# Optimization experiments

Measured on AMD Instinct MI355X. Metric: run time of the kernel, lower is better.

Reference implementation:

```python
import jax, jax.numpy as jnp
import numpy as np
import math

INF = 1e10

def setup_inputs() -> dict:
    key = jax.random.key(0)
    ks = jax.random.split(key, 6)
    B, S, T, D = 8, 1024, 1024, 1024
    stdv = 1.0 / math.sqrt(D)
    return {
        "key": jax.random.normal(ks[0], (B, S, D), dtype=jnp.float32),
        "mask_src": jnp.ones((B, S), dtype=jnp.float32),
        "mask_trg": jnp.ones((B, T), dtype=jnp.float32),
        "Wq": jax.random.uniform(ks[1], (D, D), jnp.float32, -stdv, stdv),
        "bq": jnp.zeros((D,), jnp.float32),
        "Wk": jax.random.uniform(ks[2], (D, D), jnp.float32, -stdv, stdv),
        "bk": jnp.zeros((D,), jnp.float32),
        "wg": jax.random.uniform(ks[3], (D,), jnp.float32, -stdv, stdv),
        "bg": jnp.zeros((1,), jnp.float32),
    }


def reference(key, mask_src, mask_trg, Wq, bq, Wk, bk, wg, bg):
    B, S, D = key.shape
    T = mask_trg.shape[1]
    scale = jnp.asarray(math.sqrt(D), key.dtype)

    # --- linear (position-based Gaussian) attention ---
    src_lens = mask_src.sum(-1)                      # [B]
    trg_lens = mask_trg.sum(-1)                      # [B]
    steps = src_lens / trg_lens                      # [B]
    idx_t = steps[:, None] * jnp.arange(T, dtype=key.dtype)[None, :]   # [B,T]
    idx_s = jnp.arange(S, dtype=key.dtype)                              # [S]
    dist2 = (idx_s[None, None, :] - idx_t[:, :, None]) ** 2            # [B,T,S]
    l_logits = -dist2 / 0.3 - INF * (1.0 - mask_src[:, None, :])
    l_att = jax.nn.softmax(l_logits, axis=-1)                           # [B,T,S]

    # query from position attention
    query = jnp.einsum('bts,bsd->btd', l_att, key)                      # [B,T,D]

    # learned gate, broadcast [B,T,1] -> [B,T,S]
    gates = jax.nn.sigmoid(query @ wg + bg)[:, :, None]                 # [B,T,1]

    # QK dot-product attention
    q = query @ Wq.T + bq                                               # [B,T,D]
    k = key @ Wk.T + bk                                                 # [B,S,D]
    dots = jnp.einsum('btd,bsd->bts', q, k)
    dots = dots - (1.0 - mask_src[:, None, :]) * INF
    probs = jax.nn.softmax(dots / scale, axis=-1)                       # [B,T,S]

    # gated mixture of QK attention and position attention
    return (1.0 - gates) * probs + gates * l_att
```

## Files before the change

### kernel.cpp

```cpp
#include <hip/hip_runtime.h>
#include <hip/hip_bf16.h>
#include <stdint.h>

typedef unsigned short ushort_t;

#define BB 8
#define SS 1024
#define TT 1024
#define DD 1024
#define INF_ 1e10f

__device__ __forceinline__ float b2f(ushort_t u){
  union { unsigned u32; float f; } x; x.u32 = ((unsigned)u) << 16; return x.f;
}
__device__ __forceinline__ ushort_t f2b(float f){
  union { float f; unsigned u; } x; x.f = f;
  unsigned r = x.u + 0x7FFFu + ((x.u >> 16) & 1u);
  return (ushort_t)(r >> 16);
}

__global__ __launch_bounds__(256) void pre_kernel(
    const float* __restrict__ Wq, const float* __restrict__ Wk,
    ushort_t* __restrict__ WqT, ushort_t* __restrict__ WkT,
    const float* __restrict__ msrc, const float* __restrict__ mtrg,
    float* __restrict__ steps, float* __restrict__ v2)
{
  __shared__ float tile[32][33];
  __shared__ float sh[8];
  int blk = blockIdx.x, tid = threadIdx.x;
  if (blk < 2048){
    const float* src = (blk >= 1024) ? Wk : Wq;
    ushort_t* dst = (blk >= 1024) ? WkT : WqT;
    int q = blk & 1023;
    int tx = q & 31, ty = q >> 5;
    int c = tid & 31, r0 = tid >> 5;
    #pragma unroll
    for (int k = 0; k < 4; k++){
      int r = r0 + k*8;
      tile[r][c] = src[(size_t)(ty*32 + r)*DD + tx*32 + c];
    }
    __syncthreads();
    #pragma unroll
    for (int k = 0; k < 4; k++){
      int r = r0 + k*8;
      dst[(size_t)(tx*32 + r)*DD + ty*32 + c] = f2b(tile[c][r]);
    }
  } else {
    int b = blk - 2048;
    if (b < 4) v2[b*256 + tid] = 0.f;
    float a = 0.f, c = 0.f;
    for (int i = tid; i < SS; i += 256) a += msrc[b*SS + i];
    for (int i = tid; i < TT; i += 256) c += mtrg[b*TT + i];
    #pragma unroll
    for (int o = 32; o; o >>= 1){ a += __shfl_xor(a, o); c += __shfl_xor(c, o); }
    int wv = tid >> 6, ln = tid & 63;
    if (!ln){ sh[wv] = a; sh[4+wv] = c; }
    __syncthreads();
    if (!tid){
      float sa = sh[0]+sh[1]+sh[2]+sh[3];
      float sc = sh[4]+sh[5]+sh[6]+sh[7];
      steps[b] = sa / sc;
    }
  }
}

__global__ __launch_bounds__(256) void v2_kernel(
    const float* __restrict__ Wk, const float* __restrict__ bq,
    float* __restrict__ v2)
{
  int tid = threadIdx.x;
  int f = tid * 4;
  int r0 = blockIdx.x * 32;
  float a0=0.f, a1=0.f, a2=0.f, a3=0.f;
  for (int r = 0; r < 32; r++){
    float s = bq[r0 + r];
    float4 w = *(const float4*)(Wk + (size_t)(r0 + r)*DD + f);
    a0 += s*w.x; a1 += s*w.y; a2 += s*w.z; a3 += s*w.w;
  }
  atomicAdd(&v2[f+0], a0); atomicAdd(&v2[f+1], a1);
  atomicAdd(&v2[f+2], a2); atomicAdd(&v2[f+3], a3);
}

__global__ __launch_bounds__(256) void key_convert_kernel(
    const float* __restrict__ key, const float* __restrict__ wg,
    const float* __restrict__ v2f, ushort_t* __restrict__ keyb,
    float* __restrict__ kw, float* __restrict__ cv)
{
  __shared__ float sh[8];
  int row = blockIdx.x;
  int tid = threadIdx.x, d0 = tid*4;
  float4 v = *(const float4*)(key + (size_t)row*DD + d0);
  ushort4 o; o.x=f2b(v.x); o.y=f2b(v.y); o.z=f2b(v.z); o.w=f2b(v.w);
  *(ushort4*)(keyb + (size_t)row*DD + d0) = o;
  float4 w4 = *(const float4*)(wg + d0);
  float4 u4 = *(const float4*)(v2f + d0);
  float pk = v.x*w4.x + v.y*w4.y + v.z*w4.z + v.w*w4.w;
  float pc = v.x*u4.x + v.y*u4.y + v.z*u4.z + v.w*u4.w;
  #pragma unroll
  for (int off = 32; off; off >>= 1){ pk += __shfl_xor(pk, off); pc += __shfl_xor(pc, off); }
  int wvv = tid >> 6;
  if ((tid & 63) == 0){ sh[wvv] = pk; sh[4+wvv] = pc; }
  __syncthreads();
  if (!tid){
    kw[row] = sh[0]+sh[1]+sh[2]+sh[3];
    cv[row] = sh[4]+sh[5]+sh[6]+sh[7];
  }
}

typedef __bf16 bf16x8 __attribute__((ext_vector_type(8)));
typedef float f32x4 __attribute__((ext_vector_type(4)));

#define CP16(g, l) __builtin_amdgcn_global_load_lds( \
    (const __attribute__((address_space(1))) void*)(g), \
    (__attribute__((address_space(3))) void*)(l), 16, 0, 0)

__global__ __launch_bounds__(256, 2) void gemm_bt_kernel(
    const ushort_t* __restrict__ A, const ushort_t* __restrict__ Bm,
    const float* __restrict__ bias, void* __restrict__ Cv,
    int M, int N, int K, int lda, int ldb,
    long long sA, long long sB, long long sC, int hasBias, int outBF16,
    int gx, int gxy)
{
  __shared__ ushort_t lA[128*32];
  __shared__ ushort_t lB[128*32];

  const int bpx = gridDim.x >> 3;
  const int lin = blockIdx.x;
  const int glob = (lin & 7) * bpx + (lin >> 3);
  const int bz = glob / gxy;
  const int rem = glob - bz * gxy;
  const int by = rem / gx;
  const int bx = rem - by * gx;

  A  += (size_t)bz * sA;
  Bm += (size_t)bz * sB;

  const int tid = threadIdx.x;
  const int wv = tid >> 6, ln = tid & 63;
  const int r4 = ln >> 2, c8 = (ln & 3) * 8;

  const ushort_t* gA0 = A  + (size_t)(by*128 + wv*32 + r4) * lda + c8;
  const ushort_t* gA1 = gA0 + (size_t)16 * lda;
  const ushort_t* gB0 = Bm + (size_t)(bx*128 + wv*32 + r4) * ldb + c8;
  const ushort_t* gB1 = gB0 + (size_t)16 * ldb;
  ushort_t* lA0 = &lA[(wv*32     ) * 32];
  ushort_t* lA1 = &lA[(wv*32 + 16) * 32];
  ushort_t* lB0 = &lB[(wv*32     ) * 32];
  ushort_t* lB1 = &lB[(wv*32 + 16) * 32];

  const int lm = ln & 15, qd = ln >> 4;
  const int wm = (wv >> 1) * 64, wn = (wv & 1) * 64;

  f32x4 acc[4][4];
  #pragma unroll
  for (int i = 0; i < 4; i++)
    #pragma unroll
    for (int j = 0; j < 4; j++) acc[i][j] = (f32x4){0.f, 0.f, 0.f, 0.f};

  for (int k0 = 0; k0 < K; k0 += 32){
    CP16(gA0, lA0); CP16(gA1, lA1); CP16(gB0, lB0); CP16(gB1, lB1);
    gA0 += 32; gA1 += 32; gB0 += 32; gB1 += 32;
    __syncthreads();
    bf16x8 af[4], bf[4];
    #pragma unroll
    for (int i = 0; i < 4; i++) af[i] = *(const bf16x8*)&lA[(wm + i*16 + lm)*32 + qd*8];
    #pragma unroll
    for (int j = 0; j < 4; j++) bf[j] = *(const bf16x8*)&lB[(wn + j*16 + lm)*32 + qd*8];
    #pragma unroll
    for (int i = 0; i < 4; i++)
      #pragma unroll
      for (int j = 0; j < 4; j++)
        acc[i][j] = __builtin_amdgcn_mfma_f32_16x16x32_bf16(af[i], bf[j], acc[i][j], 0, 0, 0);
    __syncthreads();
  }

  const int row0 = by*128 + wm + qd*4;
  const int col0 = bx*128 + wn + lm;
  ushort_t* Cb = (ushort_t*)Cv + (size_t)bz * sC;
  float*    Cf = (float*)Cv    + (size_t)bz * sC;
  #pragma unroll
  for (int j = 0; j < 4; j++){
    int col = col0 + j*16;
    float bv = hasBias ? bias[col] : 0.f;
    #pragma unroll
    for (int i = 0; i < 4; i++)
      #pragma unroll
      for (int r = 0; r < 4; r++){
        size_t idx = (size_t)(row0 + i*16 + r) * N + col;
        float v = acc[i][j][r] + bv;
        if (outBF16) Cb[idx] = f2b(v); else Cf[idx] = v;
      }
  }
}

#define G2_STAGE_A(sel) do{ \
    ushort_t* _d = &lA3[(sel)*(256*64) + (w*8)*64]; \
    CP16(gA0, _d); \
    CP16(gA1, _d + 64*64); \
    CP16(gA2, _d + 128*64); \
    CP16(gA3, _d + 192*64); }while(0)
#define G2_STAGE_B(sel) do{ \
    ushort_t* _d = &lB3[(sel)*(128*64) + (w*8)*64]; \
    CP16(gB0, _d); \
    CP16(gB1, _d + 64*64); }while(0)
#define G2_ADV() do{ gA0+=64; gA1+=64; gA2+=64; gA3+=64; gB0+=64; gB1+=64; }while(0)
#define BAR()    asm volatile("s_barrier" ::: "memory")
#define LGKM0()  do{ asm volatile("s_waitcnt lgkmcnt(0)" ::: "memory"); \
                     __builtin_amdgcn_sched_barrier(0); }while(0)

__global__ __launch_bounds__(512, 2) void gemm256_kernel(
    const ushort_t* __restrict__ A, const ushort_t* __restrict__ Bm,
    ushort_t* __restrict__ C,
    int M, int N, int K, int lda, int ldb,
    long long sA, long long sB, long long sC, int gx, int gxy)
{
  __shared__ ushort_t lA3[3 * 256 * 64];
  __shared__ ushort_t lB3[3 * 128 * 64];
  (void)M;

  const int bpx = gridDim.x >> 3;
  const int lin = blockIdx.x;
  const int glob = (lin & 7) * bpx + (lin >> 3);
  const int bz = glob / gxy;
  const int rem = glob - bz * gxy;
  const int by = rem / gx;
  const int bx = rem - by * gx;

  A  += (size_t)bz * sA;
  Bm += (size_t)bz * sB;

  const int tid = threadIdx.x;
  const int w = tid >> 6, l = tid & 63;
  const int lm = l & 15, qd = l >> 4;
  const int wm = w >> 2, wn = w & 3;

  const int srow = l >> 3;
  const int sch  = (l & 7) ^ srow;

  const ushort_t* gA0 = A + (size_t)(by*256 +       w*8 + srow) * lda + sch*8;
  const ushort_t* gA1 = gA0 + (size_t)64  * lda;
  const ushort_t* gA2 = gA0 + (size_t)128 * lda;
  const ushort_t* gA3 = gA0 + (size_t)192 * lda;
  const ushort_t* gB0 = Bm + (size_t)(bx*128 +      w*8 + srow) * ldb + sch*8;
  const ushort_t* gB1 = gB0 + (size_t)64  * ldb;

  f32x4 acc[8][2];
  #pragma unroll
  for (int i = 0; i < 8; i++){ acc[i][0] = (f32x4){0.f,0.f,0.f,0.f}; acc[i][1] = (f32x4){0.f,0.f,0.f,0.f}; }

  G2_STAGE_A(0); G2_STAGE_B(0); G2_ADV();
  G2_STAGE_A(1); G2_STAGE_B(1); G2_ADV();
  asm volatile("s_waitcnt vmcnt(6)" ::: "memory");
  BAR();

  const int NT = K >> 6;
  int rd = 0, st = 2;
  #pragma unroll 1
  for (int t = 0; t < NT; ++t){
    const ushort_t* sa = &lA3[rd*(256*64) + (wm*128)*64];
    const ushort_t* sb = &lB3[rd*(128*64) + (wn*32)*64];
    const bool pre = (t + 2 < NT);

    {
      const int ch = qd ^ (lm & 7);
      bf16x8 af[8], bfr[2];
      #pragma unroll
      for (int i = 0; i < 8; i++) af[i]  = *(const bf16x8*)&sa[(i*16 + lm)*64 + ch*8];
      #pragma unroll
      for (int j = 0; j < 2; j++) bfr[j] = *(const bf16x8*)&sb[(j*16 + lm)*64 + ch*8];
      if (pre) G2_STAGE_A(st);
      BAR();
      LGKM0();
      __builtin_amdgcn_s_setprio(1);
      #pragma unroll
      for (int i = 0; i < 8; i++)
        #pragma unroll
        for (int j = 0; j < 2; j++)
          acc[i][j] = __builtin_amdgcn_mfma_f32_16x16x32_bf16(af[i], bfr[j], acc[i][j], 0, 0, 0);
      __builtin_amdgcn_s_setprio(0);
      BAR();
    }
    {
      const int ch = (4 | qd) ^ (lm & 7);
      bf16x8 af[8], bfr[2];
      #pragma unroll
      for (int i = 0; i < 8; i++) af[i]  = *(const bf16x8*)&sa[(i*16 + lm)*64 + ch*8];
      #pragma unroll
      for (int j = 0; j < 2; j++) bfr[j] = *(const bf16x8*)&sb[(j*16 + lm)*64 + ch*8];
      if (pre) G2_STAGE_B(st);
      BAR();
      LGKM0();
      __builtin_amdgcn_s_setprio(1);
      #pragma unroll
      for (int i = 0; i < 8; i++)
        #pragma unroll
        for (int j = 0; j < 2; j++)
          acc[i][j] = __builtin_amdgcn_mfma_f32_16x16x32_bf16(af[i], bfr[j], acc[i][j], 0, 0, 0);
      __builtin_amdgcn_s_setprio(0);
    }
    if (pre) G2_ADV();
    if (t < NT - 1){
      if (pre) asm volatile("s_waitcnt vmcnt(6)" ::: "memory");
      else     asm volatile("s_waitcnt vmcnt(0)" ::: "memory");
      BAR();
    }
    rd = (rd == 2) ? 0 : rd + 1;
    st = (st == 2) ? 0 : st + 1;
  }

  const int row0 = by*256 + wm*128 + qd*4;
  const int col0 = bx*128 + wn*32 + lm;
  ushort_t* Cp = C + (size_t)bz * sC;
  #pragma unroll
  for (int j = 0; j < 2; j++)
    #pragma unroll
    for (int i = 0; i < 8; i++)
      #pragma unroll
      for (int r = 0; r < 4; r++)
        Cp[(size_t)(row0 + i*16 + r) * N + col0 + j*16] = f2b(acc[i][j][r]);
}

__global__ __launch_bounds__(256) void wmt_reduce_kernel(
    const float* __restrict__ part, ushort_t* __restrict__ dst)
{
  int i4 = blockIdx.x * 256 + threadIdx.x;
  const float4* p = (const float4*)part;
  float4 a = p[i4];
  float4 b = p[i4 + 262144];
  float4 c = p[i4 + 524288];
  float4 d = p[i4 + 786432];
  ushort4 o;
  o.x = f2b(a.x + b.x + c.x + d.x);
  o.y = f2b(a.y + b.y + c.y + d.y);
  o.z = f2b(a.z + b.z + c.z + d.z);
  o.w = f2b(a.w + b.w + c.w + d.w);
  ((ushort4*)dst)[i4] = o;
}

__global__ __launch_bounds__(256) void band_kernel(
    const ushort_t* __restrict__ kmb, const float* __restrict__ mask_src,
    const float* __restrict__ steps, const float* __restrict__ kw,
    const float* __restrict__ bg, ushort_t* __restrict__ qm2b,
    float* __restrict__ gates)
{
  __shared__ float shw[8][17];
  __shared__ int shslo[8];
  int bx = blockIdx.x;
  int b = bx >> 7, t0 = (bx & 127) * 8;
  int tid = threadIdx.x;

  if (tid < 8){
    int t = t0 + tid;
    float c = steps[b] * (float)t;
    int slo = (int)ceilf(c - 8.0f);
    float w[17], m = -3e38f;
    #pragma unroll
    for (int i = 0; i < 17; i++){
      int s = slo + i;
      float l = -3e38f;
      if (s >= 0 && s < SS){
        float dd = (float)s - c;
        l = -dd*dd*(1.0f/0.3f) - INF_*(1.0f - mask_src[b*SS + s]);
      }
      w[i] = l; m = fmaxf(m, l);
    }
    float norm = 0.f, ga = 0.f;
    #pragma unroll
    for (int i = 0; i < 17; i++){
      float e = __expf(w[i] - m);
      int s = slo + i;
      if (s >= 0 && s < SS) ga += e * kw[b*SS + s]; else e = 0.f;
      w[i] = e; norm += e;
    }
    float inv = 1.0f / norm;
    #pragma unroll
    for (int i = 0; i < 17; i++) shw[tid][i] = w[i] * inv;
    shslo[tid] = slo;
    gates[b*TT + t] = 1.0f / (1.0f + __expf(-(ga*inv + bg[0])));
  }
  __syncthreads();

  int smin = shslo[0], smax = shslo[7] + 16;
  if (smin < 0) smin = 0;
  if (smax > SS-1) smax = SS-1;
  int d0 = tid * 4;
  float acc[8][4];
  #pragma unroll
  for (int t = 0; t < 8; t++){ acc[t][0]=0.f; acc[t][1]=0.f; acc[t][2]=0.f; acc[t][3]=0.f; }

  const ushort_t* kbase = kmb + ((size_t)b*SS)*DD + d0;
  for (int s = smin; s <= smax; s++){
    ushort4 kv = *(const ushort4*)(kbase + (size_t)s*DD);
    float k0 = b2f(kv.x), k1 = b2f(kv.y), k2 = b2f(kv.z), k3 = b2f(kv.w);
    #pragma unroll
    for (int t = 0; t < 8; t++){
      unsigned u = (unsigned)(s - shslo[t]);
      if (u < 17u){
        float wgt = shw[t][u];
        acc[t][0] += wgt*k0; acc[t][1] += wgt*k1; acc[t][2] += wgt*k2; acc[t][3] += wgt*k3;
      }
    }
  }
  #pragma unroll
  for (int t = 0; t < 8; t++){
    ushort4 o; o.x=f2b(acc[t][0]); o.y=f2b(acc[t][1]); o.z=f2b(acc[t][2]); o.w=f2b(acc[t][3]);
    *(ushort4*)(qm2b + ((size_t)(b*TT + t0 + t))*DD + d0) = o;
  }
}

__device__ __forceinline__ float blkmax(float v, float* sh){
  #pragma unroll
  for (int o = 32; o; o >>= 1) v = fmaxf(v, __shfl_xor(v, o));
  __syncthreads();
  if ((threadIdx.x & 63) == 0) sh[threadIdx.x >> 6] = v;
  __syncthreads();
  return fmaxf(fmaxf(sh[0], sh[1]), fmaxf(sh[2], sh[3]));
}
__device__ __forceinline__ float blksum(float v, float* sh){
  #pragma unroll
  for (int o = 32; o; o >>= 1) v += __shfl_xor(v, o);
  __syncthreads();
  if ((threadIdx.x & 63) == 0) sh[threadIdx.x >> 6] = v;
  __syncthreads();
  return sh[0] + sh[1] + sh[2] + sh[3];
}

__global__ __launch_bounds__(256) void softmax_mix_kernel(
    const ushort_t* __restrict__ dotsb, float* __restrict__ out,
    const float* __restrict__ mask_src, const float* __restrict__ steps,
    const float* __restrict__ gates, const float* __restrict__ cv)
{
  __shared__ float sh[4];
  int blk = blockIdx.x;
  int b = blk >> 10, t = blk & 1023;
  int tid = threadIdx.x;
  int s0 = tid * 4;
  float c = steps[b] * (float)t;

  ushort4 dv = *(const ushort4*)(dotsb + (size_t)blk*SS + s0);
  float4 mv = *(const float4*)(mask_src + (size_t)b*SS + s0);
  float4 cva = *(const float4*)(cv + (size_t)b*SS + s0);
  float dvf[4] = {b2f(dv.x) + cva.x, b2f(dv.y) + cva.y, b2f(dv.z) + cva.z, b2f(dv.w) + cva.w};
  float msk[4] = {mv.x, mv.y, mv.z, mv.w};
  float dl[4], ll[4];
  float dmax = -3e38f, lmax = -3e38f;
  #pragma unroll
  for (int r = 0; r < 4; r++){
    float im = INF_ * (1.0f - msk[r]);
    dl[r] = (dvf[r] - im) * (1.0f/32.0f);
    float dd = (float)(s0 + r) - c;
    ll[r] = -dd*dd*(1.0f/0.3f) - im;
    dmax = fmaxf(dmax, dl[r]);
    lmax = fmaxf(lmax, ll[r]);
  }
  float dm = blkmax(dmax, sh);
  float ps[4], lp[4];
  float psum = 0.f, lsum = 0.f;
  #pragma unroll
  for (int r = 0; r < 4; r++){ ps[r] = __expf(dl[r] - dm); psum += ps[r]; }
  psum = blksum(psum, sh);
  float lm2 = blkmax(lmax, sh);
  #pragma unroll
  for (int r = 0; r < 4; r++){ lp[r] = __expf(ll[r] - lm2); lsum += lp[r]; }
  lsum = blksum(lsum, sh);

  float g = gates[blk];
  float ip = (1.0f - g) / psum, il = g / lsum;
  float4 ov;
  ov.x = ps[0]*ip + lp[0]*il;
  ov.y = ps[1]*ip + lp[1]*il;
  ov.z = ps[2]*ip + lp[2]*il;
  ov.w = ps[3]*ip + lp[3]*il;
  *(float4*)(out + (size_t)blk*SS + s0) = ov;
}

extern "C" void kernel_launch(void* const* d_in, const int* in_sizes, int n_in,
                              void* d_out, int out_size, void* d_ws, size_t ws_size,
                              hipStream_t stream)
{
  const float* key      = (const float*)d_in[0];
  const float* mask_src = (const float*)d_in[1];
  const float* mask_trg = (const float*)d_in[2];
  const float* Wq       = (const float*)d_in[3];
  const float* bq       = (const float*)d_in[4];
  const float* Wk       = (const float*)d_in[5];
  const float* bk       = (const float*)d_in[6];
  const float* wg       = (const float*)d_in[7];
  const float* bg       = (const float*)d_in[8];
  float* out = (float*)d_out;
  (void)bk;

  char* ws = (char*)d_ws;
  float* steps     = (float*)ws;
  float* gates     = (float*)(ws + 4096);
  float* cv        = (float*)(ws + 4096 + 32768);
  float* kw        = (float*)(ws + 4096 + 65536);
  float* v2        = (float*)(ws + 4096 + 98304);
  ushort_t* WqTb   = (ushort_t*)(ws + 131072);
  ushort_t* WkTb   = WqTb + (size_t)DD*DD;
  ushort_t* WmTb   = WkTb + (size_t)DD*DD;
  ushort_t* keyb   = WmTb + (size_t)DD*DD;
  ushort_t* kmb    = keyb + (size_t)BB*SS*DD;
  char* shared16   = (char*)(kmb + (size_t)BB*SS*DD);
  float* wmPart    = (float*)shared16;
  ushort_t* qm2b   = (ushort_t*)shared16;
  ushort_t* dotsb  = kmb;

  pre_kernel<<<2056, 256, 0, stream>>>(Wq, Wk, WqTb, WkTb, mask_src, mask_trg, steps, v2);
  v2_kernel<<<32, 256, 0, stream>>>(Wk, bq, v2);
  key_convert_kernel<<<BB*SS, 256, 0, stream>>>(key, wg, v2, keyb, kw, cv);
  gemm_bt_kernel<<<256, 256, 0, stream>>>(
      WkTb, WqTb, nullptr, (void*)wmPart, DD, DD, DD/4, DD, DD,
      DD/4, DD/4, (long long)DD*DD, 0, 0, 8, 64);
  wmt_reduce_kernel<<<DD*DD/4/256, 256, 0, stream>>>(wmPart, WmTb);
  gemm256_kernel<<<256, 512, 0, stream>>>(
      keyb, WmTb, kmb, BB*SS, DD, DD, DD, DD, 0, 0, 0, 8, 256);
  band_kernel<<<BB*TT/8, 256, 0, stream>>>(kmb, mask_src, steps, kw, bg, qm2b, gates);
  gemm256_kernel<<<256, 512, 0, stream>>>(
      qm2b, keyb, dotsb, TT, SS, DD, DD, DD,
      (long long)TT*DD, (long long)SS*DD, (long long)TT*SS, 8, 32);
  softmax_mix_kernel<<<BB*TT, 256, 0, stream>>>(dotsb, out, mask_src, steps, gates, cv);
}
```

Before: 211.8 us.

## Merge small prep kernels, reorder block mapping, and fuse softmax reductions

```diff
diff --git a/kernel.cpp b/kernel.cpp
--- a/kernel.cpp
+++ b/kernel.cpp
@@ -23,10 +23,12 @@
     const float* __restrict__ Wq, const float* __restrict__ Wk,
     ushort_t* __restrict__ WqT, ushort_t* __restrict__ WkT,
     const float* __restrict__ msrc, const float* __restrict__ mtrg,
-    float* __restrict__ steps, float* __restrict__ v2)
+    float* __restrict__ steps, float* __restrict__ v2,
+    const float* __restrict__ bq)
 {
   __shared__ float tile[32][33];
   __shared__ float sh[8];
+  __shared__ float shv[128];
   int blk = blockIdx.x, tid = threadIdx.x;
   if (blk < 2048){
     const float* src = (blk >= 1024) ? Wk : Wq;
@@ -45,9 +47,8 @@
       int r = r0 + k*8;
       dst[(size_t)(tx*32 + r)*DD + ty*32 + c] = f2b(tile[c][r]);
     }
-  } else {
+  } else if (blk < 2056){
     int b = blk - 2048;
-    if (b < 4) v2[b*256 + tid] = 0.f;
     float a = 0.f, c = 0.f;
     for (int i = tid; i < SS; i += 256) a += msrc[b*SS + i];
     for (int i = tid; i < TT; i += 256) c += mtrg[b*TT + i];
@@ -61,33 +62,43 @@
       float sc = sh[4]+sh[5]+sh[6]+sh[7];
       steps[b] = sa / sc;
     }
-  }
-}
-
-__global__ __launch_bounds__(256) void v2_kernel(
-    const float* __restrict__ Wk, const float* __restrict__ bq,
-    float* __restrict__ v2)
-{
-  int tid = threadIdx.x;
-  int f = tid * 4;
-  int r0 = blockIdx.x * 32;
-  float a0=0.f, a1=0.f, a2=0.f, a3=0.f;
-  for (int r = 0; r < 32; r++){
-    float s = bq[r0 + r];
-    float4 w = *(const float4*)(Wk + (size_t)(r0 + r)*DD + f);
-    a0 += s*w.x; a1 += s*w.y; a2 += s*w.z; a3 += s*w.w;
-  }
-  atomicAdd(&v2[f+0], a0); atomicAdd(&v2[f+1], a1);
-  atomicAdd(&v2[f+2], a2); atomicAdd(&v2[f+3], a3);
+  } else {
+    int b2 = blk - 2056;
+    int fcol = b2*128 + (tid & 127);
+    int half = tid >> 7;
+    float a = 0.f;
+    const float* Wp = Wk + (size_t)(half*512)*DD + fcol;
+    for (int d = 0; d < 512; ++d) a += Wp[(size_t)d*DD] * bq[half*512 + d];
+    if (half == 0) shv[tid] = a;
+    __syncthreads();
+    if (half == 1) v2[fcol] = a + shv[tid & 127];
+  }
 }
 
 __global__ __launch_bounds__(256) void key_convert_kernel(
     const float* __restrict__ key, const float* __restrict__ wg,
     const float* __restrict__ v2f, ushort_t* __restrict__ keyb,
-    float* __restrict__ kw, float* __restrict__ cv)
+    float* __restrict__ kw, float* __restrict__ cv,
+    const float* __restrict__ part, ushort_t* __restrict__ wmt)
 {
   __shared__ float sh[8];
-  int row = blockIdx.x;
+  int blk = blockIdx.x;
+  if (blk >= BB*SS){
+    int i4 = (blk - BB*SS) * 256 + threadIdx.x;
+    const float4* p = (const float4*)part;
+    float4 a = p[i4];
+    float4 b = p[i4 + 262144];
+    float4 c = p[i4 + 524288];
+    float4 d = p[i4 + 786432];
+    ushort4 o;
+    o.x = f2b(a.x + b.x + c.x + d.x);
+    o.y = f2b(a.y + b.y + c.y + d.y);
+    o.z = f2b(a.z + b.z + c.z + d.z);
+    o.w = f2b(a.w + b.w + c.w + d.w);
+    ((ushort4*)wmt)[i4] = o;
+    return;
+  }
+  int row = blk;
   int tid = threadIdx.x, d0 = tid*4;
   float4 v = *(const float4*)(key + (size_t)row*DD + d0);
   ushort4 o; o.x=f2b(v.x); o.y=f2b(v.y); o.z=f2b(v.z); o.w=f2b(v.w);
@@ -320,23 +331,6 @@
         Cp[(size_t)(row0 + i*16 + r) * N + col0 + j*16] = f2b(acc[i][j][r]);
 }
 
-__global__ __launch_bounds__(256) void wmt_reduce_kernel(
-    const float* __restrict__ part, ushort_t* __restrict__ dst)
-{
-  int i4 = blockIdx.x * 256 + threadIdx.x;
-  const float4* p = (const float4*)part;
-  float4 a = p[i4];
-  float4 b = p[i4 + 262144];
-  float4 c = p[i4 + 524288];
-  float4 d = p[i4 + 786432];
-  ushort4 o;
-  o.x = f2b(a.x + b.x + c.x + d.x);
-  o.y = f2b(a.y + b.y + c.y + d.y);
-  o.z = f2b(a.z + b.z + c.z + d.z);
-  o.w = f2b(a.w + b.w + c.w + d.w);
-  ((ushort4*)dst)[i4] = o;
-}
-
 __global__ __launch_bounds__(256) void band_kernel(
     const ushort_t* __restrict__ kmb, const float* __restrict__ mask_src,
     const float* __restrict__ steps, const float* __restrict__ kw,
@@ -345,7 +339,8 @@
 {
   __shared__ float shw[8][17];
   __shared__ int shslo[8];
-  int bx = blockIdx.x;
+  int bx0 = blockIdx.x;
+  int bx = (bx0 & 7) * 128 + (bx0 >> 3);
   int b = bx >> 7, t0 = (bx & 127) * 8;
   int tid = threadIdx.x;
 
@@ -408,21 +403,29 @@
   }
 }
 
-__device__ __forceinline__ float blkmax(float v, float* sh){
-  #pragma unroll
-  for (int o = 32; o; o >>= 1) v = fmaxf(v, __shfl_xor(v, o));
+__device__ __forceinline__ void blkmax2(float& v1, float& v2, float* sh8){
+  #pragma unroll
+  for (int o = 32; o; o >>= 1){
+    v1 = fmaxf(v1, __shfl_xor(v1, o));
+    v2 = fmaxf(v2, __shfl_xor(v2, o));
+  }
+  int wv = threadIdx.x >> 6;
+  if ((threadIdx.x & 63) == 0){ sh8[wv] = v1; sh8[4+wv] = v2; }
   __syncthreads();
-  if ((threadIdx.x & 63) == 0) sh[threadIdx.x >> 6] = v;
+  v1 = fmaxf(fmaxf(sh8[0], sh8[1]), fmaxf(sh8[2], sh8[3]));
+  v2 = fmaxf(fmaxf(sh8[4], sh8[5]), fmaxf(sh8[6], sh8[7]));
+}
+__device__ __forceinline__ void blksum2(float& v1, float& v2, float* sh8){
+  #pragma unroll
+  for (int o = 32; o; o >>= 1){
+    v1 += __shfl_xor(v1, o);
+    v2 += __shfl_xor(v2, o);
+  }
+  int wv = threadIdx.x >> 6;
+  if ((threadIdx.x & 63) == 0){ sh8[wv] = v1; sh8[4+wv] = v2; }
   __syncthreads();
-  return fmaxf(fmaxf(sh[0], sh[1]), fmaxf(sh[2], sh[3]));
-}
-__device__ __forceinline__ float blksum(float v, float* sh){
-  #pragma unroll
-  for (int o = 32; o; o >>= 1) v += __shfl_xor(v, o);
-  __syncthreads();
-  if ((threadIdx.x & 63) == 0) sh[threadIdx.x >> 6] = v;
-  __syncthreads();
-  return sh[0] + sh[1] + sh[2] + sh[3];
+  v1 = sh8[0]+sh8[1]+sh8[2]+sh8[3];
+  v2 = sh8[4]+sh8[5]+sh8[6]+sh8[7];
 }
 
 __global__ __launch_bounds__(256) void softmax_mix_kernel(
@@ -430,8 +433,10 @@
     const float* __restrict__ mask_src, const float* __restrict__ steps,
     const float* __restrict__ gates, const float* __restrict__ cv)
 {
-  __shared__ float sh[4];
-  int blk = blockIdx.x;
+  __shared__ float shA[8];
+  __shared__ float shB[8];
+  int blk0 = blockIdx.x;
+  int blk = (blk0 & 7) * 1024 + (blk0 >> 3);
   int b = blk >> 10, t = blk & 1023;
   int tid = threadIdx.x;
   int s0 = tid * 4;
@@ -453,16 +458,15 @@
     dmax = fmaxf(dmax, dl[r]);
     lmax = fmaxf(lmax, ll[r]);
   }
-  float dm = blkmax(dmax, sh);
+  blkmax2(dmax, lmax, shA);
   float ps[4], lp[4];
   float psum = 0.f, lsum = 0.f;
   #pragma unroll
-  for (int r = 0; r < 4; r++){ ps[r] = __expf(dl[r] - dm); psum += ps[r]; }
-  psum = blksum(psum, sh);
-  float lm2 = blkmax(lmax, sh);
-  #pragma unroll
-  for (int r = 0; r < 4; r++){ lp[r] = __expf(ll[r] - lm2); lsum += lp[r]; }
-  lsum = blksum(lsum, sh);
+  for (int r = 0; r < 4; r++){
+    ps[r] = __expf(dl[r] - dmax); psum += ps[r];
+    lp[r] = __expf(ll[r] - lmax); lsum += lp[r];
+  }
+  blksum2(psum, lsum, shB);
 
   float g = gates[blk];
   float ip = (1.0f - g) / psum, il = g / lsum;
@@ -506,13 +510,12 @@
   ushort_t* qm2b   = (ushort_t*)shared16;
   ushort_t* dotsb  = kmb;
 
-  pre_kernel<<<2056, 256, 0, stream>>>(Wq, Wk, WqTb, WkTb, mask_src, mask_trg, steps, v2);
-  v2_kernel<<<32, 256, 0, stream>>>(Wk, bq, v2);
-  key_convert_kernel<<<BB*SS, 256, 0, stream>>>(key, wg, v2, keyb, kw, cv);
+  pre_kernel<<<2064, 256, 0, stream>>>(Wq, Wk, WqTb, WkTb, mask_src, mask_trg, steps, v2, bq);
   gemm_bt_kernel<<<256, 256, 0, stream>>>(
       WkTb, WqTb, nullptr, (void*)wmPart, DD, DD, DD/4, DD, DD,
       DD/4, DD/4, (long long)DD*DD, 0, 0, 8, 64);
-  wmt_reduce_kernel<<<DD*DD/4/256, 256, 0, stream>>>(wmPart, WmTb);
+  key_convert_kernel<<<BB*SS + 1024, 256, 0, stream>>>(
+      key, wg, v2, keyb, kw, cv, wmPart, WmTb);
   gemm256_kernel<<<256, 512, 0, stream>>>(
       keyb, WmTb, kmb, BB*SS, DD, DD, DD, DD, 0, 0, 0, 8, 256);
   band_kernel<<<BB*TT/8, 256, 0, stream>>>(kmb, mask_src, steps, kw, bg, qm2b, gates);
```

Measured after the change: 212.0 us. Within noise of the previous version (+0.1%).
